# Kernel optimization log

Measured on AMD Instinct MI355X. Metric: run time of the kernel, lower is better.

Reference implementation:

```python
import jax, jax.numpy as jnp
import numpy as np

B, N, E, C, K, D, L, FC, IN, OUT = 2, 40000, 320000, 128, 64, 2, 4, 128, 3, 1


def _gelu(x):
    return jax.nn.gelu(x, approximate=False)  # torch F.gelu default = exact erf


def _compute_gradient(f, tgt, src, egw):
    # f: [B,C,N]; tgt,src: [B,E] int; egw: [B,E,D] -> returns [B, C*D, N]
    fT = f.transpose(0, 2, 1)  # [B,N,C]
    diff = jnp.take_along_axis(fT, src[..., None], axis=1) - jnp.take_along_axis(fT, tgt[..., None], axis=1)  # [B,E,C]
    msg = (diff[:, :, :, None] * egw[:, :, None, :]).reshape(fT.shape[0], tgt.shape[1], -1)  # [B,E,C*D], c outer / d inner
    g = jnp.zeros((fT.shape[0], fT.shape[1], msg.shape[-1]), f.dtype)
    g = g.at[jnp.arange(fT.shape[0])[:, None], tgt].add(msg)  # scatter_add over target nodes
    return g.transpose(0, 2, 1)


def _spectral(x, wc, ws, w0, bc, bs, b0, wbc, wbs, wb0):
    # x: [B,Cin,N]; wc/ws: [Cin,Cout,K]; w0: [Cin,Cout,1]; bases: [B,N,K] or [B,N,1]
    xc = jnp.einsum('bix,bxk->bik', x, wbc)
    xs = -jnp.einsum('bix,bxk->bik', x, wbs)
    x0 = jnp.einsum('bix,bxk->bik', x, wb0)
    fc = jnp.einsum('bik,iok->bok', xc, wc) - jnp.einsum('bik,iok->bok', xs, ws)
    fs = jnp.einsum('bik,iok->bok', xs, wc) + jnp.einsum('bik,iok->bok', xc, ws)
    f0 = jnp.einsum('bik,iok->bok', x0, w0)
    return (jnp.einsum('bok,bxk->box', f0, b0)
            + 2.0 * jnp.einsum('bok,bxk->box', fc, bc)
            - 2.0 * jnp.einsum('bok,bxk->box', fs, bs))


def _forward(x, node_mask, nodes, node_weights, edge_gradient_weights, modes,
             fc0_w, fc0_b, sp_wc, sp_ws, sp_w0, w_w, w_b, gw_w, gw_b,
             fc1_w, fc1_b, fc2_w, fc2_b, directed_edges):
    temp = jnp.einsum('bxd,kd->bxk', nodes, modes)
    bc = jnp.cos(temp) * node_mask
    bs = jnp.sin(temp) * node_mask
    b0 = node_mask
    wbc, wbs, wb0 = bc * node_weights, bs * node_weights, b0 * node_weights
    h = (x @ fc0_w + fc0_b).transpose(0, 2, 1)  # lift -> [B,C,N]
    tgt = directed_edges[..., 0]
    src = directed_edges[..., 1]
    nl = sp_wc.shape[0]
    for i in range(nl):
        x1 = _spectral(h, sp_wc[i], sp_ws[i], sp_w0[i], bc, bs, b0, wbc, wbs, wb0)
        x2 = jnp.einsum('oc,bcn->bon', w_w[i], h) + w_b[i][None, :, None]  # 1x1 conv
        # x3 is computed but NOT added, exactly matching the source (x = x1 + x2)
        x3 = jnp.einsum('oc,bcn->bon', gw_w[i],
                        jax.nn.soft_sign(_compute_gradient(h, tgt, src, edge_gradient_weights))) + gw_b[i][None, :, None]
        h = x1 + x2
        if i != nl - 1:
            h = _gelu(h)
    h = h.transpose(0, 2, 1)  # [B,N,C]
    h = _gelu(h @ fc1_w + fc1_b)
    return h @ fc2_w + fc2_b  # [B,N,OUT]


def setup_inputs() -> dict:
    key = jax.random.key(0)
    ks = jax.random.split(key, 16)
    scale = 1.0 / float(C * C)
    return {
        'x': jax.random.normal(ks[0], (B, N, IN), jnp.float32),
        'node_mask': jnp.ones((B, N, 1), jnp.float32),
        'nodes': jax.random.uniform(ks[1], (B, N, D), jnp.float32),
        'node_weights': jax.random.uniform(ks[2], (B, N, 1), jnp.float32) * (1.0 / N),
        'directed_edges': jax.random.randint(ks[3], (B, E, 2), 0, N, dtype=jnp.int32),
        'edge_gradient_weights': jax.random.normal(ks[4], (B, E, D), jnp.float32) * 0.1,
        'modes': jax.random.normal(ks[5], (K, D), jnp.float32) * 4.0,
        'fc0_w': jax.random.normal(ks[6], (IN, C), jnp.float32) * float(1.0 / np.sqrt(IN)),
        'fc0_b': jnp.zeros((C,), jnp.float32),
        'sp_wc': jax.random.uniform(ks[7], (L, C, C, K), jnp.float32) * scale,
        'sp_ws': jax.random.uniform(ks[8], (L, C, C, K), jnp.float32) * scale,
        'sp_w0': jax.random.uniform(ks[9], (L, C, C, 1), jnp.float32) * scale,
        'w_w': jax.random.normal(ks[10], (L, C, C), jnp.float32) * float(1.0 / np.sqrt(C)),
        'w_b': jnp.zeros((L, C), jnp.float32),
        'gw_w': jax.random.normal(ks[11], (L, C, D * C), jnp.float32) * float(1.0 / np.sqrt(D * C)),
        'gw_b': jnp.zeros((L, C), jnp.float32),
        'fc1_w': jax.random.normal(ks[12], (C, FC), jnp.float32) * float(1.0 / np.sqrt(C)),
        'fc1_b': jnp.zeros((FC,), jnp.float32),
        'fc2_w': jax.random.normal(ks[13], (FC, OUT), jnp.float32) * float(1.0 / np.sqrt(FC)),
        'fc2_b': jnp.zeros((OUT,), jnp.float32),
    }


def reference(x, node_mask, nodes, node_weights, directed_edges, edge_gradient_weights, modes,
              fc0_w, fc0_b, sp_wc, sp_ws, sp_w0, w_w, w_b, gw_w, gw_b,
              fc1_w, fc1_b, fc2_w, fc2_b):
    return _forward(x, node_mask, nodes, node_weights, edge_gradient_weights, modes,
                    fc0_w, fc0_b, sp_wc, sp_ws, sp_w0, w_w, w_b, gw_w, gw_b,
                    fc1_w, fc1_b, fc2_w, fc2_b, directed_edges)
```

## Files before the change

### kernel.cpp

```cpp
#include <hip/hip_runtime.h>
#include <math.h>

#define NN 40000
#define NP 40064
#define CC 128
#define KK 64
#define BATCH 2
#define NLAYER 4
#define FSPLITS 128
#define MODES 144
#define KTOT 256
#define NCH 626

typedef __attribute__((ext_vector_type(8))) short bf16x8;
typedef __attribute__((ext_vector_type(4))) float f32x4;
typedef __attribute__((ext_vector_type(4))) unsigned short u16x4;
typedef __attribute__((ext_vector_type(8))) unsigned short u16x8;

__device__ __forceinline__ float gelu_exact(float x) {
    return 0.5f * x * (1.0f + erff(x * 0.70710678118654752f));
}
__device__ __forceinline__ unsigned short f2bf(float x) {
    unsigned int u = __float_as_uint(x);
    u += 0x7FFFu + ((u >> 16) & 1u);
    return (unsigned short)(u >> 16);
}

__global__ __launch_bounds__(256) void basis_kernel(
        const float* __restrict__ nodes, const float* __restrict__ mask,
        const float* __restrict__ wts, const float* __restrict__ modes,
        unsigned short* __restrict__ Binv, float* __restrict__ maskp,
        float* __restrict__ warr) {
    __shared__ float sm[KK * 2];
    int t = threadIdx.x;
    if (t < KK * 2) sm[t] = modes[t];
    __syncthreads();
    int idx = blockIdx.x * 256 + t;
    int b = idx / NP, n = idx - b * NP;
    float nx = 0.f, ny = 0.f, m = 0.f, w = 0.f;
    if (n < NN) {
        long gi = (long)b * NN + n;
        nx = nodes[gi * 2]; ny = nodes[gi * 2 + 1];
        m = mask[gi]; w = wts[gi];
    }
    unsigned int bcp[32], bsp[32];
    #pragma unroll
    for (int k2 = 0; k2 < 32; ++k2) {
        float t0 = nx * sm[4 * k2]     + ny * sm[4 * k2 + 1];
        float t1 = nx * sm[4 * k2 + 2] + ny * sm[4 * k2 + 3];
        float s0, c0, s1, c1;
        __sincosf(t0, &s0, &c0);
        __sincosf(t1, &s1, &c1);
        bcp[k2] = (unsigned int)f2bf(c0 * m) | ((unsigned int)f2bf(c1 * m) << 16);
        bsp[k2] = (unsigned int)f2bf(s0 * m) | ((unsigned int)f2bf(s1 * m) << 16);
    }
    maskp[idx] = m;
    warr[idx]  = w;
    uint4* brow = (uint4*)(Binv + (long)idx * KTOT);
    #pragma unroll
    for (int q = 0; q < 8; ++q)
        brow[q] = make_uint4(bcp[4*q], bcp[4*q+1], bcp[4*q+2], bcp[4*q+3]);
    #pragma unroll
    for (int q = 0; q < 8; ++q)
        brow[8 + q] = make_uint4(bsp[4*q], bsp[4*q+1], bsp[4*q+2], bsp[4*q+3]);
}

__global__ void fc1t_kernel(const float* __restrict__ fc1, unsigned short* __restrict__ fc1t) {
    int idx = blockIdx.x * 256 + threadIdx.x;
    int f = idx >> 7, c = idx & 127;
    fc1t[f * 128 + c] = f2bf(fc1[c * 128 + f]);
}

__global__ __launch_bounds__(512) void lift_fused(const float* __restrict__ x,
        const float* __restrict__ w, const float* __restrict__ bvec,
        unsigned short* __restrict__ Binv, const float* __restrict__ warr,
        const float* __restrict__ maskp, float* __restrict__ pxcs) {
    int s = blockIdx.x, b = blockIdx.y;
    int t = threadIdx.x, wv = t >> 6, l = t & 63, lo = l & 15, hi = l >> 4;
    __shared__ __align__(16) char lds[52480];
    char* Btile = lds;
    char* Ts    = lds;
    char* Ts2   = lds + 16384;
    char* Wt    = lds + 32768;
    float* xl   = (float*)(lds + 51200);
    float* wl   = (float*)(lds + 51968);
    float* ml   = (float*)(lds + 52224);
    int c = t & 127, ng = t >> 7;
    float w0 = w[c], w1 = w[CC + c], w2 = w[2 * CC + c], bv = bvec[c];
    f32x4 accF[9];
    #pragma unroll
    for (int mt = 0; mt < 9; ++mt) accF[mt] = (f32x4){0.f, 0.f, 0.f, 0.f};
    const char* Bbase = (const char*)Binv + (long)b * NP * 512;
    if (t < 480) *(unsigned int*)(Wt + 129 * 128 + t * 4) = 0u;

    int lrow = t >> 3, lcol = (t & 7) * 32;
    uint4 pB0 = {}, pB1 = {};
    float pxv = 0.f, pwv = 0.f, pmv = 0.f;
    {
        const char* Bsrc = Bbase + (long)s * 64 * 512;
        pB0 = *(const uint4*)(Bsrc + (long)lrow * 512 + lcol);
        pB1 = *(const uint4*)(Bsrc + (long)lrow * 512 + lcol + 16);
        if (t < 192) pxv = x[((long)b * NN + s * 64) * 3 + t];
        if (t < 64) { pwv = warr[(long)b * NP + s * 64 + t]; pmv = maskp[(long)b * NP + s * 64 + t]; }
    }

    for (int chunk = s; chunk < NCH; chunk += FSPLITS) {
        int nbase = chunk * 64;
        __syncthreads();
        {
            int a0 = lrow * 256 + lcol;
            int key = (lrow & 7) << 4;
            *(uint4*)(Btile + (a0 ^ key)) = pB0;
            *(uint4*)(Btile + ((a0 + 16) ^ key)) = pB1;
            if (t < 192) xl[t] = pxv;
            if (t < 64) { wl[t] = pwv; ml[t] = pmv; }
        }
        int nc = chunk + FSPLITS;
        if (nc < NCH) {
            const char* Bsrc = Bbase + (long)nc * 64 * 512;
            pB0 = *(const uint4*)(Bsrc + (long)lrow * 512 + lcol);
            pB1 = *(const uint4*)(Bsrc + (long)lrow * 512 + lcol + 16);
            if (nc * 64 < NN && t < 192) pxv = x[((long)b * NN + nc * 64) * 3 + t];
            if (t < 64) { pwv = warr[(long)b * NP + nc * 64 + t]; pmv = maskp[(long)b * NP + nc * 64 + t]; }
        }
        __syncthreads();
        {
            int g = t >> 6, n_ = t & 63;
            int rkey = (n_ & 7) << 4;
            int raddr = n_ * 256 + g * 32;
            u16x8 r0 = *(const u16x8*)(Btile + (raddr ^ rkey));
            u16x8 r1 = *(const u16x8*)(Btile + ((raddr + 16) ^ rkey));
            #pragma unroll
            for (int i = 0; i < 8; ++i) {
                int mr = g * 16 + i;
                *(unsigned short*)(Wt + ((mr * 128 + n_ * 2) ^ ((mr & 7) << 4))) = r0[i];
            }
            #pragma unroll
            for (int i = 0; i < 8; ++i) {
                int mr = g * 16 + 8 + i;
                *(unsigned short*)(Wt + ((mr * 128 + n_ * 2) ^ ((mr & 7) << 4))) = r1[i];
            }
            if (t < 64) *(unsigned short*)(Wt + 128 * 128 + t * 2) = f2bf(ml[t]);
        }
        __syncthreads();
        {
            u16x8 hv0, hv1;
            #pragma unroll
            for (int j = 0; j < 16; ++j) {
                int n = ng * 16 + j;
                float h = 0.f;
                if (nbase < NN) h = bv + xl[n * 3] * w0 + xl[n * 3 + 1] * w1 + xl[n * 3 + 2] * w2;
                unsigned short hb = f2bf(h);
                unsigned short hwb = f2bf(h * wl[n]);
                if (j < 8) hv0[j] = hwb; else hv1[j - 8] = hwb;
                *(unsigned short*)(Ts + (((n << 8) + c * 2) ^ ((n & 7) << 4))) = hb;
            }
            int base2 = c * 128 + ng * 32;
            *(u16x8*)(Ts2 + (base2 ^ ((c & 7) << 4))) = hv0;
            *(u16x8*)(Ts2 + ((base2 + 16) ^ ((c & 7) << 4))) = hv1;
        }
        __syncthreads();
        char* Bdst = (char*)Binv + ((long)b * NP + nbase) * 512 + 256;
        #pragma unroll
        for (int pass = 0; pass < 2; ++pass) {
            int n = pass * 32 + (t >> 4), seg = t & 15;
            uint4 v = *(const uint4*)(Ts + (((n << 8) + (seg << 4)) ^ ((n & 7) << 4)));
            *(uint4*)(Bdst + (long)n * 512 + seg * 16) = v;
        }
        int ct = wv * 16;
        #pragma unroll
        for (int ks2 = 0; ks2 < 2; ++ks2) {
            int ar = ct + lo;
            bf16x8 a = *(const bf16x8*)(Ts2 + ((ar * 128 + ks2 * 64 + hi * 16) ^ ((ar & 7) << 4)));
            #pragma unroll
            for (int mt = 0; mt < 9; ++mt) {
                int mrow = mt * 16 + lo;
                bf16x8 bb = *(const bf16x8*)(Wt + ((mrow * 128 + ks2 * 64 + hi * 16) ^ ((mrow & 7) << 4)));
                accF[mt] = __builtin_amdgcn_mfma_f32_16x16x32_bf16(a, bb, accF[mt], 0, 0, 0);
            }
        }
    }
    float* pb = pxcs + ((long)s * BATCH + b) * CC * MODES;
    #pragma unroll
    for (int mt = 0; mt < 9; ++mt)
        #pragma unroll
        for (int r = 0; r < 4; ++r)
            pb[(long)(wv * 16 + hi * 4 + r) * MODES + mt * 16 + lo] = accF[mt][r];
}

__global__ __launch_bounds__(256) void reduce_kernel(const float* __restrict__ pxcs,
        float* __restrict__ xc, float* __restrict__ xs, float* __restrict__ x0) {
    int gid = blockIdx.x * 256 + threadIdx.x;
    int idx = gid >> 3, sg = gid & 7;
    float a = 0.f;
    #pragma unroll
    for (int j = 0; j < 16; ++j)
        a += pxcs[(long)(sg * 16 + j) * (BATCH * CC * MODES) + idx];
    a += __shfl_xor(a, 1); a += __shfl_xor(a, 2); a += __shfl_xor(a, 4);
    if (sg == 0) {
        int m = idx % MODES, bc_ = idx / MODES;
        if (m < 64)        xc[bc_ * KK + m] = a;
        else if (m < 128)  xs[bc_ * KK + m - 64] = a;
        else if (m == 128) x0[bc_] = a;
    }
}

__global__ __launch_bounds__(1024) void mix_kernel(const float* __restrict__ xc,
        const float* __restrict__ xs, const float* __restrict__ x0,
        const float* __restrict__ wc, const float* __restrict__ wsp,
        const float* __restrict__ w0, const float* __restrict__ ww,
        const float* __restrict__ wbias, unsigned short* __restrict__ A,
        float* __restrict__ f0a, float* __restrict__ wba, int layer) {
    int o = blockIdx.x, b = blockIdx.y;
    int k = threadIdx.x & 63, ig = threadIdx.x >> 6;
    const float* wcl = wc  + (long)layer * CC * CC * KK;
    const float* wsl = wsp + (long)layer * CC * CC * KK;
    float fc = 0.f, fs = 0.f;
    #pragma unroll
    for (int j = 0; j < 8; ++j) {
        int i = ig * 8 + j;
        float xci = xc[(b * CC + i) * KK + k];
        float xsi = xs[(b * CC + i) * KK + k];
        float wcv = wcl[((long)i * CC + o) * KK + k];
        float wsv = wsl[((long)i * CC + o) * KK + k];
        fc += xci * wcv + xsi * wsv;
        fs += xci * wsv - xsi * wcv;
    }
    __shared__ float rc[16][64], rs[16][64];
    rc[ig][k] = fc; rs[ig][k] = fs;
    __syncthreads();
    unsigned short* Ar = A + ((long)b * CC + o) * KTOT;
    if (ig == 0) {
        fc = 0.f; fs = 0.f;
        #pragma unroll
        for (int j = 0; j < 16; ++j) { fc += rc[j][k]; fs += rs[j][k]; }
        Ar[k]      = f2bf(2.f * fc);
        Ar[64 + k] = f2bf(-2.f * fs);
    } else if (ig == 1) {
        const float* wwl = ww + ((long)layer * CC + o) * CC;
        Ar[128 + k] = f2bf(wwl[k]);
        Ar[192 + k] = f2bf(wwl[64 + k]);
    } else if (ig == 2) {
        const float* w0l = w0 + (long)layer * CC * CC;
        float p = x0[b * CC + k] * w0l[(long)k * CC + o]
                + x0[b * CC + 64 + k] * w0l[(long)(64 + k) * CC + o];
        #pragma unroll
        for (int off = 32; off > 0; off >>= 1) p += __shfl_down(p, off, 64);
        if (k == 0) { f0a[b * CC + o] = p; wba[b * CC + o] = wbias[layer * CC + o]; }
    }
}

template <int DO_FWD, int DOGELU>
__global__ __launch_bounds__(512) void fused_inv(const unsigned short* __restrict__ Amat,
        unsigned short* Binv, const float* __restrict__ f0a, const float* __restrict__ wba,
        const float* __restrict__ maskp, const float* __restrict__ warr,
        float* __restrict__ pxcs) {
    int s = blockIdx.x, b = blockIdx.y;
    int t = threadIdx.x, wv = t >> 6, l = t & 63, lo = l & 15, hi = l >> 4;
    __shared__ __align__(16) char lds[51712];
    char* Btile = lds;
    char* Ts    = lds;
    char* Ts2   = lds + 16384;
    char* Wt    = lds + 32768;
    float* ml   = (float*)(lds + 51200);
    float* wl   = (float*)(lds + 51456);
    const unsigned short* Ab = Amat + (long)b * CC * KTOT;
    bf16x8 af[8];
    {
        const unsigned short* arow = Ab + (long)(wv * 16 + lo) * KTOT + hi * 8;
        #pragma unroll
        for (int ks = 0; ks < 8; ++ks) af[ks] = *(const bf16x8*)(arow + ks * 32);
    }
    int o0 = wv * 16 + hi * 4;
    f32x4 f0v = *(const f32x4*)(f0a + b * CC + o0);
    f32x4 wbv = *(const f32x4*)(wba + b * CC + o0);
    int swz = (lo & 7) << 4;
    f32x4 accF[9];
    #pragma unroll
    for (int mt = 0; mt < 9; ++mt) accF[mt] = (f32x4){0.f, 0.f, 0.f, 0.f};
    const char* Bbase = (const char*)Binv + (long)b * NP * 512;
    if (DO_FWD && t < 480) *(unsigned int*)(Wt + 129 * 128 + t * 4) = 0u;

    uint4 pB0 = {}, pB1 = {}, pB2 = {}, pB3 = {};
    float pmv = 0.f, pwv = 0.f;
    {
        const char* Bsrc = Bbase + (long)s * 64 * 512;
        pB0 = *(const uint4*)(Bsrc + 0 * 8192 + t * 16);
        pB1 = *(const uint4*)(Bsrc + 1 * 8192 + t * 16);
        pB2 = *(const uint4*)(Bsrc + 2 * 8192 + t * 16);
        pB3 = *(const uint4*)(Bsrc + 3 * 8192 + t * 16);
        if (t < 64) { pmv = maskp[(long)b * NP + s * 64 + t]; pwv = warr[(long)b * NP + s * 64 + t]; }
    }

    for (int chunk = s; chunk < NCH; chunk += FSPLITS) {
        int nbase = chunk * 64;
        __syncthreads();
        {
            int o = 0 * 8192 + t * 16; *(uint4*)(Btile + (o ^ (((o >> 9) & 7) << 4))) = pB0;
            o = 1 * 8192 + t * 16;     *(uint4*)(Btile + (o ^ (((o >> 9) & 7) << 4))) = pB1;
            o = 2 * 8192 + t * 16;     *(uint4*)(Btile + (o ^ (((o >> 9) & 7) << 4))) = pB2;
            o = 3 * 8192 + t * 16;     *(uint4*)(Btile + (o ^ (((o >> 9) & 7) << 4))) = pB3;
            if (t < 64) { ml[t] = pmv; wl[t] = pwv; }
        }
        int nc = chunk + FSPLITS;
        if (nc < NCH) {
            const char* Bsrc = Bbase + (long)nc * 64 * 512;
            pB0 = *(const uint4*)(Bsrc + 0 * 8192 + t * 16);
            pB1 = *(const uint4*)(Bsrc + 1 * 8192 + t * 16);
            pB2 = *(const uint4*)(Bsrc + 2 * 8192 + t * 16);
            pB3 = *(const uint4*)(Bsrc + 3 * 8192 + t * 16);
            if (t < 64) { pmv = maskp[(long)b * NP + nc * 64 + t]; pwv = warr[(long)b * NP + nc * 64 + t]; }
        }
        __syncthreads();
        if (DO_FWD) {
            int g = t >> 6, n_ = t & 63;
            int rkey = (n_ & 7) << 4;
            int raddr = n_ * 512 + g * 32;
            u16x8 r0 = *(const u16x8*)(Btile + (raddr ^ rkey));
            u16x8 r1 = *(const u16x8*)(Btile + ((raddr + 16) ^ rkey));
            #pragma unroll
            for (int i = 0; i < 8; ++i) {
                int mr = g * 16 + i;
                *(unsigned short*)(Wt + ((mr * 128 + n_ * 2) ^ ((mr & 7) << 4))) = r0[i];
            }
            #pragma unroll
            for (int i = 0; i < 8; ++i) {
                int mr = g * 16 + 8 + i;
                *(unsigned short*)(Wt + ((mr * 128 + n_ * 2) ^ ((mr & 7) << 4))) = r1[i];
            }
            if (t < 64) *(unsigned short*)(Wt + 128 * 128 + t * 2) = f2bf(ml[t]);
        }
        f32x4 acc[4];
        #pragma unroll
        for (int fn = 0; fn < 4; ++fn) acc[fn] = (f32x4){0.f, 0.f, 0.f, 0.f};
        #pragma unroll
        for (int ks = 0; ks < 8; ++ks) {
            #pragma unroll
            for (int fn = 0; fn < 4; ++fn) {
                int boff = ((fn * 16 + lo) << 9) + (ks << 6) + (hi << 4);
                bf16x8 bb = *(const bf16x8*)(Btile + (boff ^ swz));
                acc[fn] = __builtin_amdgcn_mfma_f32_16x16x32_bf16(af[ks], bb, acc[fn], 0, 0, 0);
            }
        }
        __syncthreads();
        #pragma unroll
        for (int fn = 0; fn < 4; ++fn) {
            int n = fn * 16 + lo;
            float mv = ml[n];
            u16x4 pk;
            #pragma unroll
            for (int r = 0; r < 4; ++r) {
                float v = acc[fn][r] + f0v[r] * mv + wbv[r];
                if (DOGELU) v = gelu_exact(v);
                pk[r] = f2bf(v);
                if (DO_FWD)
                    *(unsigned short*)(Ts2 + (((o0 + r) * 128 + n * 2) ^ (((o0 + r) & 7) << 4))) = f2bf(v * wl[n]);
            }
            *(u16x4*)(Ts + (((n << 8) + (o0 << 1)) ^ ((n & 7) << 4))) = pk;
        }
        __syncthreads();
        char* Bdst = (char*)Binv + ((long)b * NP + nbase) * 512 + 256;
        #pragma unroll
        for (int pass = 0; pass < 2; ++pass) {
            int n = pass * 32 + (t >> 4), seg = t & 15;
            uint4 v = *(const uint4*)(Ts + (((n << 8) + (seg << 4)) ^ ((n & 7) << 4)));
            *(uint4*)(Bdst + (long)n * 512 + seg * 16) = v;
        }
        if (DO_FWD) {
            int ct = wv * 16;
            #pragma unroll
            for (int ks2 = 0; ks2 < 2; ++ks2) {
                int ar = ct + lo;
                bf16x8 a = *(const bf16x8*)(Ts2 + ((ar * 128 + ks2 * 64 + hi * 16) ^ ((ar & 7) << 4)));
                #pragma unroll
                for (int mt = 0; mt < 9; ++mt) {
                    int mrow = mt * 16 + lo;
                    bf16x8 bb = *(const bf16x8*)(Wt + ((mrow * 128 + ks2 * 64 + hi * 16) ^ ((mrow & 7) << 4)));
                    accF[mt] = __builtin_amdgcn_mfma_f32_16x16x32_bf16(a, bb, accF[mt], 0, 0, 0);
                }
            }
        }
    }
    if (DO_FWD) {
        float* pb = pxcs + ((long)s * BATCH + b) * CC * MODES;
        #pragma unroll
        for (int mt = 0; mt < 9; ++mt)
            #pragma unroll
            for (int r = 0; r < 4; ++r)
                pb[(long)(wv * 16 + hi * 4 + r) * MODES + mt * 16 + lo] = accF[mt][r];
    }
}

__global__ __launch_bounds__(256) void head_mfma(const unsigned short* __restrict__ Binv,
        const unsigned short* __restrict__ fc1t, const float* __restrict__ b1,
        const float* __restrict__ fc2, const float* __restrict__ b2, float* __restrict__ out) {
    int t = threadIdx.x, wv = t >> 6, l = t & 63, lo = l & 15, hi = l >> 4;
    int b = blockIdx.y;
    int nb = (blockIdx.x * 4 + wv) * 16;
    const unsigned short* Arow = Binv + ((long)b * NP + nb + lo) * KTOT + 128 + hi * 8;
    f32x4 acc[8];
    #pragma unroll
    for (int ft = 0; ft < 8; ++ft) acc[ft] = (f32x4){0.f, 0.f, 0.f, 0.f};
    #pragma unroll
    for (int ks = 0; ks < 4; ++ks) {
        bf16x8 a = *(const bf16x8*)(Arow + ks * 32);
        #pragma unroll
        for (int ft = 0; ft < 8; ++ft) {
            bf16x8 bv = *(const bf16x8*)(fc1t + (ft * 16 + lo) * 128 + ks * 32 + hi * 8);
            acc[ft] = __builtin_amdgcn_mfma_f32_16x16x32_bf16(a, bv, acc[ft], 0, 0, 0);
        }
    }
    float s[4] = {0.f, 0.f, 0.f, 0.f};
    #pragma unroll
    for (int ft = 0; ft < 8; ++ft) {
        int f = ft * 16 + lo;
        float b1f = b1[f], f2f = fc2[f];
        #pragma unroll
        for (int r = 0; r < 4; ++r) s[r] += gelu_exact(acc[ft][r] + b1f) * f2f;
    }
    float b2v = b2[0];
    #pragma unroll
    for (int r = 0; r < 4; ++r) {
        float v = s[r];
        v += __shfl_xor(v, 1); v += __shfl_xor(v, 2);
        v += __shfl_xor(v, 4); v += __shfl_xor(v, 8);
        if (lo == 0) out[(long)b * NN + nb + hi * 4 + r] = v + b2v;
    }
}

extern "C" void kernel_launch(void* const* d_in, const int* in_sizes, int n_in,
                              void* d_out, int out_size, void* d_ws, size_t ws_size,
                              hipStream_t stream) {
    const float* x     = (const float*)d_in[0];
    const float* mask  = (const float*)d_in[1];
    const float* nodes = (const float*)d_in[2];
    const float* wts   = (const float*)d_in[3];
    const float* modes = (const float*)d_in[6];
    const float* fc0w  = (const float*)d_in[7];
    const float* fc0b  = (const float*)d_in[8];
    const float* spwc  = (const float*)d_in[9];
    const float* spws  = (const float*)d_in[10];
    const float* spw0  = (const float*)d_in[11];
    const float* ww    = (const float*)d_in[12];
    const float* wb    = (const float*)d_in[13];
    const float* fc1w  = (const float*)d_in[16];
    const float* fc1b  = (const float*)d_in[17];
    const float* fc2w  = (const float*)d_in[18];
    const float* fc2b  = (const float*)d_in[19];

    char* p = (char*)d_ws;
    auto alloc = [&](size_t bytes) { char* r = p; p += (bytes + 255) & ~255UL; return r; };
    unsigned short* Binv = (unsigned short*)alloc((size_t)BATCH * NP * KTOT * 2);
    unsigned short* Amat = (unsigned short*)alloc((size_t)BATCH * CC * KTOT * 2);
    unsigned short* fc1t = (unsigned short*)alloc((size_t)CC * 128 * 2);
    float* pxcs = (float*)alloc((size_t)FSPLITS * BATCH * CC * MODES * 4);
    float* xcb  = (float*)alloc((size_t)BATCH * CC * KK * 4);
    float* xsb  = (float*)alloc((size_t)BATCH * CC * KK * 4);
    float* x0b  = (float*)alloc((size_t)BATCH * CC * 4);
    float* f0a  = (float*)alloc((size_t)BATCH * CC * 4);
    float* wba  = (float*)alloc((size_t)BATCH * CC * 4);
    float* maskp = (float*)alloc((size_t)BATCH * NP * 4);
    float* warr  = (float*)alloc((size_t)BATCH * NP * 4);

    basis_kernel<<<(BATCH * NP) / 256, 256, 0, stream>>>(nodes, mask, wts, modes, Binv, maskp, warr);
    fc1t_kernel<<<64, 256, 0, stream>>>(fc1w, fc1t);
    lift_fused<<<dim3(FSPLITS, BATCH), 512, 0, stream>>>(x, fc0w, fc0b, Binv, warr, maskp, pxcs);

    for (int l = 0; l < NLAYER; ++l) {
        reduce_kernel<<<(8 * BATCH * CC * MODES) / 256, 256, 0, stream>>>(pxcs, xcb, xsb, x0b);
        mix_kernel<<<dim3(CC, BATCH), 1024, 0, stream>>>(xcb, xsb, x0b, spwc, spws, spw0,
                                                         ww, wb, Amat, f0a, wba, l);
        if (l < NLAYER - 1)
            fused_inv<1, 1><<<dim3(FSPLITS, BATCH), 512, 0, stream>>>(
                Amat, Binv, f0a, wba, maskp, warr, pxcs);
        else
            fused_inv<0, 0><<<dim3(FSPLITS, BATCH), 512, 0, stream>>>(
                Amat, Binv, f0a, wba, maskp, warr, pxcs);
    }
    head_mfma<<<dim3(NN / 64, BATCH), 256, 0, stream>>>(Binv, fc1t, fc1b, fc2w, fc2b, (float*)d_out);
}
```

Baseline: 206.3 us.

## Fuse basis computation into lift kernel and store split partials in bf16

```diff
diff --git a/kernel.cpp b/kernel.cpp
--- a/kernel.cpp
+++ b/kernel.cpp
@@ -25,44 +25,8 @@
     u += 0x7FFFu + ((u >> 16) & 1u);
     return (unsigned short)(u >> 16);
 }
-
-__global__ __launch_bounds__(256) void basis_kernel(
-        const float* __restrict__ nodes, const float* __restrict__ mask,
-        const float* __restrict__ wts, const float* __restrict__ modes,
-        unsigned short* __restrict__ Binv, float* __restrict__ maskp,
-        float* __restrict__ warr) {
-    __shared__ float sm[KK * 2];
-    int t = threadIdx.x;
-    if (t < KK * 2) sm[t] = modes[t];
-    __syncthreads();
-    int idx = blockIdx.x * 256 + t;
-    int b = idx / NP, n = idx - b * NP;
-    float nx = 0.f, ny = 0.f, m = 0.f, w = 0.f;
-    if (n < NN) {
-        long gi = (long)b * NN + n;
-        nx = nodes[gi * 2]; ny = nodes[gi * 2 + 1];
-        m = mask[gi]; w = wts[gi];
-    }
-    unsigned int bcp[32], bsp[32];
-    #pragma unroll
-    for (int k2 = 0; k2 < 32; ++k2) {
-        float t0 = nx * sm[4 * k2]     + ny * sm[4 * k2 + 1];
-        float t1 = nx * sm[4 * k2 + 2] + ny * sm[4 * k2 + 3];
-        float s0, c0, s1, c1;
-        __sincosf(t0, &s0, &c0);
-        __sincosf(t1, &s1, &c1);
-        bcp[k2] = (unsigned int)f2bf(c0 * m) | ((unsigned int)f2bf(c1 * m) << 16);
-        bsp[k2] = (unsigned int)f2bf(s0 * m) | ((unsigned int)f2bf(s1 * m) << 16);
-    }
-    maskp[idx] = m;
-    warr[idx]  = w;
-    uint4* brow = (uint4*)(Binv + (long)idx * KTOT);
-    #pragma unroll
-    for (int q = 0; q < 8; ++q)
-        brow[q] = make_uint4(bcp[4*q], bcp[4*q+1], bcp[4*q+2], bcp[4*q+3]);
-    #pragma unroll
-    for (int q = 0; q < 8; ++q)
-        brow[8 + q] = make_uint4(bsp[4*q], bsp[4*q+1], bsp[4*q+2], bsp[4*q+3]);
+__device__ __forceinline__ float bf2f(unsigned short v) {
+    return __uint_as_float(((unsigned int)v) << 16);
 }
 
 __global__ void fc1t_kernel(const float* __restrict__ fc1, unsigned short* __restrict__ fc1t) {
@@ -73,83 +37,84 @@
 
 __global__ __launch_bounds__(512) void lift_fused(const float* __restrict__ x,
         const float* __restrict__ w, const float* __restrict__ bvec,
-        unsigned short* __restrict__ Binv, const float* __restrict__ warr,
-        const float* __restrict__ maskp, float* __restrict__ pxcs) {
+        const float* __restrict__ nodes, const float* __restrict__ mask,
+        const float* __restrict__ wts, const float* __restrict__ modes,
+        unsigned short* __restrict__ Binv, float* __restrict__ maskp,
+        float* __restrict__ warr, unsigned short* __restrict__ pxcs) {
     int s = blockIdx.x, b = blockIdx.y;
     int t = threadIdx.x, wv = t >> 6, l = t & 63, lo = l & 15, hi = l >> 4;
-    __shared__ __align__(16) char lds[52480];
-    char* Btile = lds;
-    char* Ts    = lds;
-    char* Ts2   = lds + 16384;
-    char* Wt    = lds + 32768;
-    float* xl   = (float*)(lds + 51200);
-    float* wl   = (float*)(lds + 51968);
-    float* ml   = (float*)(lds + 52224);
+    __shared__ __align__(16) char lds[53504];
+    char* Ts   = lds;
+    char* Ts2  = lds + 16384;
+    char* Wt   = lds + 32768;
+    float* xl  = (float*)(lds + 51200);
+    float* ndl = (float*)(lds + 51968);
+    float* wl  = (float*)(lds + 52480);
+    float* ml  = (float*)(lds + 52736);
+    float* sm  = (float*)(lds + 52992);
     int c = t & 127, ng = t >> 7;
     float w0 = w[c], w1 = w[CC + c], w2 = w[2 * CC + c], bv = bvec[c];
     f32x4 accF[9];
     #pragma unroll
     for (int mt = 0; mt < 9; ++mt) accF[mt] = (f32x4){0.f, 0.f, 0.f, 0.f};
-    const char* Bbase = (const char*)Binv + (long)b * NP * 512;
+    if (t < 128) sm[t] = modes[t];
     if (t < 480) *(unsigned int*)(Wt + 129 * 128 + t * 4) = 0u;
 
-    int lrow = t >> 3, lcol = (t & 7) * 32;
-    uint4 pB0 = {}, pB1 = {};
-    float pxv = 0.f, pwv = 0.f, pmv = 0.f;
-    {
-        const char* Bsrc = Bbase + (long)s * 64 * 512;
-        pB0 = *(const uint4*)(Bsrc + (long)lrow * 512 + lcol);
-        pB1 = *(const uint4*)(Bsrc + (long)lrow * 512 + lcol + 16);
-        if (t < 192) pxv = x[((long)b * NN + s * 64) * 3 + t];
-        if (t < 64) { pwv = warr[(long)b * NP + s * 64 + t]; pmv = maskp[(long)b * NP + s * 64 + t]; }
-    }
+    auto fetch = [&](int chunk) -> float {
+        int nbase = chunk * 64;
+        if (nbase >= NN) return 0.f;
+        long base = (long)b * NN + nbase;
+        if (t < 192) return x[base * 3 + t];
+        if (t < 320) return nodes[base * 2 + (t - 192)];
+        if (t < 384) return wts[base + (t - 320)];
+        if (t < 448) return mask[base + (t - 384)];
+        return 0.f;
+    };
+    float pf = fetch(s);
 
     for (int chunk = s; chunk < NCH; chunk += FSPLITS) {
         int nbase = chunk * 64;
         __syncthreads();
         {
-            int a0 = lrow * 256 + lcol;
-            int key = (lrow & 7) << 4;
-            *(uint4*)(Btile + (a0 ^ key)) = pB0;
-            *(uint4*)(Btile + ((a0 + 16) ^ key)) = pB1;
-            if (t < 192) xl[t] = pxv;
-            if (t < 64) { wl[t] = pwv; ml[t] = pmv; }
+            if (t < 192)      xl[t] = pf;
+            else if (t < 320) ndl[t - 192] = pf;
+            else if (t < 384) wl[t - 320] = pf;
+            else if (t < 448) ml[t - 384] = pf;
         }
         int nc = chunk + FSPLITS;
-        if (nc < NCH) {
-            const char* Bsrc = Bbase + (long)nc * 64 * 512;
-            pB0 = *(const uint4*)(Bsrc + (long)lrow * 512 + lcol);
-            pB1 = *(const uint4*)(Bsrc + (long)lrow * 512 + lcol + 16);
-            if (nc * 64 < NN && t < 192) pxv = x[((long)b * NN + nc * 64) * 3 + t];
-            if (t < 64) { pwv = warr[(long)b * NP + nc * 64 + t]; pmv = maskp[(long)b * NP + nc * 64 + t]; }
-        }
+        if (nc < NCH) pf = fetch(nc);
         __syncthreads();
         {
-            int g = t >> 6, n_ = t & 63;
-            int rkey = (n_ & 7) << 4;
-            int raddr = n_ * 256 + g * 32;
-            u16x8 r0 = *(const u16x8*)(Btile + (raddr ^ rkey));
-            u16x8 r1 = *(const u16x8*)(Btile + ((raddr + 16) ^ rkey));
-            #pragma unroll
-            for (int i = 0; i < 8; ++i) {
-                int mr = g * 16 + i;
-                *(unsigned short*)(Wt + ((mr * 128 + n_ * 2) ^ ((mr & 7) << 4))) = r0[i];
-            }
-            #pragma unroll
-            for (int i = 0; i < 8; ++i) {
-                int mr = g * 16 + 8 + i;
-                *(unsigned short*)(Wt + ((mr * 128 + n_ * 2) ^ ((mr & 7) << 4))) = r1[i];
-            }
-            if (t < 64) *(unsigned short*)(Wt + 128 * 128 + t * 2) = f2bf(ml[t]);
-        }
-        __syncthreads();
+            int n_ = t & 63, g = t >> 6;
+            float nx = ndl[n_ * 2], ny = ndl[n_ * 2 + 1];
+            float m = ml[n_];
+            u16x8 cosr, sinr;
+            #pragma unroll
+            for (int j = 0; j < 8; ++j) {
+                int k = g * 8 + j;
+                float tv = nx * sm[2 * k] + ny * sm[2 * k + 1];
+                float sv, cv;
+                __sincosf(tv, &sv, &cv);
+                unsigned short cb = f2bf(cv * m), sb = f2bf(sv * m);
+                cosr[j] = cb; sinr[j] = sb;
+                *(unsigned short*)(Wt + ((k * 128 + n_ * 2) ^ ((k & 7) << 4))) = cb;
+                *(unsigned short*)(Wt + (((64 + k) * 128 + n_ * 2) ^ (((64 + k) & 7) << 4))) = sb;
+            }
+            char* brow = (char*)Binv + ((long)b * NP + nbase + n_) * 512 + g * 16;
+            *(u16x8*)brow = cosr;
+            *(u16x8*)(brow + 128) = sinr;
+            if (t < 64) {
+                *(unsigned short*)(Wt + 128 * 128 + n_ * 2) = f2bf(m);
+                maskp[(long)b * NP + nbase + n_] = m;
+                warr[(long)b * NP + nbase + n_] = wl[n_];
+            }
+        }
         {
             u16x8 hv0, hv1;
             #pragma unroll
             for (int j = 0; j < 16; ++j) {
                 int n = ng * 16 + j;
-                float h = 0.f;
-                if (nbase < NN) h = bv + xl[n * 3] * w0 + xl[n * 3 + 1] * w1 + xl[n * 3 + 2] * w2;
+                float h = bv + xl[n * 3] * w0 + xl[n * 3 + 1] * w1 + xl[n * 3 + 2] * w2;
                 unsigned short hb = f2bf(h);
                 unsigned short hwb = f2bf(h * wl[n]);
                 if (j < 8) hv0[j] = hwb; else hv1[j - 8] = hwb;
@@ -180,22 +145,22 @@
             }
         }
     }
-    float* pb = pxcs + ((long)s * BATCH + b) * CC * MODES;
+    unsigned short* pb = pxcs + ((long)s * BATCH + b) * CC * MODES;
     #pragma unroll
     for (int mt = 0; mt < 9; ++mt)
         #pragma unroll
         for (int r = 0; r < 4; ++r)
-            pb[(long)(wv * 16 + hi * 4 + r) * MODES + mt * 16 + lo] = accF[mt][r];
-}
-
-__global__ __launch_bounds__(256) void reduce_kernel(const float* __restrict__ pxcs,
+            pb[(long)(wv * 16 + hi * 4 + r) * MODES + mt * 16 + lo] = f2bf(accF[mt][r]);
+}
+
+__global__ __launch_bounds__(256) void reduce_kernel(const unsigned short* __restrict__ pxcs,
         float* __restrict__ xc, float* __restrict__ xs, float* __restrict__ x0) {
     int gid = blockIdx.x * 256 + threadIdx.x;
     int idx = gid >> 3, sg = gid & 7;
     float a = 0.f;
     #pragma unroll
     for (int j = 0; j < 16; ++j)
-        a += pxcs[(long)(sg * 16 + j) * (BATCH * CC * MODES) + idx];
+        a += bf2f(pxcs[(long)(sg * 16 + j) * (BATCH * CC * MODES) + idx]);
     a += __shfl_xor(a, 1); a += __shfl_xor(a, 2); a += __shfl_xor(a, 4);
     if (sg == 0) {
         int m = idx % MODES, bc_ = idx / MODES;
@@ -254,7 +219,7 @@
 __global__ __launch_bounds__(512) void fused_inv(const unsigned short* __restrict__ Amat,
         unsigned short* Binv, const float* __restrict__ f0a, const float* __restrict__ wba,
         const float* __restrict__ maskp, const float* __restrict__ warr,
-        float* __restrict__ pxcs) {
+        unsigned short* __restrict__ pxcs) {
     int s = blockIdx.x, b = blockIdx.y;
     int t = threadIdx.x, wv = t >> 6, l = t & 63, lo = l & 15, hi = l >> 4;
     __shared__ __align__(16) char lds[51712];
@@ -382,12 +347,12 @@
         }
     }
     if (DO_FWD) {
-        float* pb = pxcs + ((long)s * BATCH + b) * CC * MODES;
+        unsigned short* pb = pxcs + ((long)s * BATCH + b) * CC * MODES;
         #pragma unroll
         for (int mt = 0; mt < 9; ++mt)
             #pragma unroll
             for (int r = 0; r < 4; ++r)
-                pb[(long)(wv * 16 + hi * 4 + r) * MODES + mt * 16 + lo] = accF[mt][r];
+                pb[(long)(wv * 16 + hi * 4 + r) * MODES + mt * 16 + lo] = f2bf(accF[mt][r]);
     }
 }
 
@@ -453,7 +418,7 @@
     unsigned short* Binv = (unsigned short*)alloc((size_t)BATCH * NP * KTOT * 2);
     unsigned short* Amat = (unsigned short*)alloc((size_t)BATCH * CC * KTOT * 2);
     unsigned short* fc1t = (unsigned short*)alloc((size_t)CC * 128 * 2);
-    float* pxcs = (float*)alloc((size_t)FSPLITS * BATCH * CC * MODES * 4);
+    unsigned short* pxcs = (unsigned short*)alloc((size_t)FSPLITS * BATCH * CC * MODES * 2);
     float* xcb  = (float*)alloc((size_t)BATCH * CC * KK * 4);
     float* xsb  = (float*)alloc((size_t)BATCH * CC * KK * 4);
     float* x0b  = (float*)alloc((size_t)BATCH * CC * 4);
@@ -462,9 +427,9 @@
     float* maskp = (float*)alloc((size_t)BATCH * NP * 4);
     float* warr  = (float*)alloc((size_t)BATCH * NP * 4);
 
-    basis_kernel<<<(BATCH * NP) / 256, 256, 0, stream>>>(nodes, mask, wts, modes, Binv, maskp, warr);
     fc1t_kernel<<<64, 256, 0, stream>>>(fc1w, fc1t);
-    lift_fused<<<dim3(FSPLITS, BATCH), 512, 0, stream>>>(x, fc0w, fc0b, Binv, warr, maskp, pxcs);
+    lift_fused<<<dim3(FSPLITS, BATCH), 512, 0, stream>>>(x, fc0w, fc0b, nodes, mask, wts,
+                                                         modes, Binv, maskp, warr, pxcs);
 
     for (int l = 0; l < NLAYER; ++l) {
         reduce_kernel<<<(8 * BATCH * CC * MODES) / 256, 256, 0, stream>>>(pxcs, xcb, xsb, x0b);
```

Result: faster. 197.2 us (-4.4%).
